# Kernel tuning notes

Measured on AMD Instinct MI355X. Metric: run time of the kernel, lower is better.

Reference implementation:

```python
import jax, jax.numpy as jnp
import numpy as np

FILTERS = 64
HIDDEN = 128
T_PRED = 24
DILATIONS = (1, 2, 4, 8, 16, 32)
N_DIL = len(DILATIONS)
FEAT = 15
B = 1024
L_ENC = 168


def setup_inputs() -> dict:
    key = jax.random.key(0)
    ks = jax.random.split(key, 16)
    s = 0.05
    d_in = 1 + FEAT  # prev_output (1) concat current feature
    inp = {
        "decoder_features": jax.random.normal(ks[0], (B, T_PRED, FEAT), jnp.float32),
        "decoder_init_input": jax.random.normal(ks[1], (B, 1), jnp.float32),
        "encoder_states": jax.random.normal(ks[2], (N_DIL, B, L_ENC, FILTERS), jnp.float32),
        # dense_1: d_in -> filters (tanh)
        "W1": jax.random.normal(ks[3], (d_in, FILTERS), jnp.float32) * s,
        "b1": jnp.zeros((FILTERS,), jnp.float32),
        # dense_2: filters -> 2*filters (bias)
        "W2": jax.random.normal(ks[4], (FILTERS, 2 * FILTERS), jnp.float32) * s,
        "b2": jnp.zeros((2 * FILTERS,), jnp.float32),
        # dense_3: filters -> 2*filters (no bias)
        "W3": jax.random.normal(ks[5], (FILTERS, 2 * FILTERS), jnp.float32) * s,
        # dense_4: filters -> 2*filters (bias)
        "W4": jax.random.normal(ks[6], (FILTERS, 2 * FILTERS), jnp.float32) * s,
        "b4": jnp.zeros((2 * FILTERS,), jnp.float32),
        # dense_5: n_dil*filters -> hidden (relu)
        "W5": jax.random.normal(ks[7], (N_DIL * FILTERS, HIDDEN), jnp.float32) * s,
        "b5": jnp.zeros((HIDDEN,), jnp.float32),
        # dense_6: hidden -> 1
        "W6": jax.random.normal(ks[8], (HIDDEN, 1), jnp.float32) * s,
        "b6": jnp.zeros((1,), jnp.float32),
    }
    return inp


def _decode(decoder_features, decoder_init_input, encoder_states,
            W1, b1, W2, b2, W3, W4, b4, W5, b5, W6, b6):
    L = encoder_states.shape[2]
    # 'appended' holds the inputs written back into each dilation's state
    # (the growing-concat part of encoder_states in the original loop).
    appended0 = jnp.zeros((N_DIL, decoder_features.shape[0], T_PRED, FILTERS),
                          dtype=decoder_features.dtype)

    def step(carry, t):
        prev, appended = carry
        cur = jnp.concatenate([prev, decoder_features[:, t, :]], axis=1)  # [B, 1+FEAT]
        inputs = jnp.tanh(cur @ W1 + b1)  # [B, F]
        skips_list = []
        for i, d in enumerate(DILATIONS):
            # grown-state read index is (L + t) - d; if t >= d it lands in the
            # appended region (step t-d), otherwise in the original encoder state.
            idx_app = jnp.clip(t - d, 0, T_PRED - 1)
            idx_orig = jnp.clip(L + t - d, 0, L - 1)
            st_app = jax.lax.dynamic_index_in_dim(appended[i], idx_app, axis=1, keepdims=False)
            st_orig = jax.lax.dynamic_index_in_dim(encoder_states[i], idx_orig, axis=1, keepdims=False)
            state = jnp.where(t >= d, st_app, st_orig)  # [B, F]
            dilated = state @ W2 + b2 + inputs @ W3  # [B, 2F]
            conv_filter, conv_gate = dilated[:, :FILTERS], dilated[:, FILTERS:]
            gated = jnp.tanh(conv_filter) * jax.nn.sigmoid(conv_gate)
            out = gated @ W4 + b4  # [B, 2F]
            skips, residuals = out[:, :FILTERS], out[:, FILTERS:]
            inputs = inputs + residuals
            appended = appended.at[i, :, t, :].set(inputs)
            skips_list.append(skips)
        skip = jax.nn.relu(jnp.concatenate(skips_list, axis=1))  # [B, N_DIL*F]
        h = jax.nn.relu(skip @ W5 + b5)
        y = h @ W6 + b6  # [B, 1]
        return (y, appended), y

    (_, _), ys = jax.lax.scan(step, (decoder_init_input, appended0),
                              jnp.arange(T_PRED))
    return jnp.transpose(ys, (1, 0, 2))  # [B, T, 1]


def reference(decoder_features, decoder_init_input, encoder_states,
              W1, b1, W2, b2, W3, W4, b4, W5, b5, W6, b6):
    return _decode(decoder_features, decoder_init_input, encoder_states,
                   W1, b1, W2, b2, W3, W4, b4, W5, b5, W6, b6)
```

## Files before the change

### kernel.cpp

```cpp
#include <hip/hip_runtime.h>

typedef _Float16 h16;
typedef _Float16 half4 __attribute__((ext_vector_type(4)));
typedef _Float16 half8 __attribute__((ext_vector_type(8)));
typedef float floatx4 __attribute__((ext_vector_type(4)));

#define B_TOT 1024
#define T_STEPS 24
#define F 64
#define C2 128
#define FEAT 15
#define L_ENC 168
#define HID 128
#define R 16
#define BLK 256
#define FP 72

__device__ __forceinline__ floatx4 mfma16(half8 a, half8 b, floatx4 c) {
  return __builtin_amdgcn_mfma_f32_16x16x32_f16(a, b, c, 0, 0, 0);
}

#define BAR() asm volatile("s_waitcnt lgkmcnt(0)\n\ts_barrier" ::: "memory")

__device__ __forceinline__ float tanh_fast(float x) {
  float cx = fminf(fmaxf(x, -15.f), 15.f);
  float e  = __builtin_amdgcn_exp2f(-2.885390081777927f * cx);
  return (1.f - e) * __builtin_amdgcn_rcpf(1.f + e);
}
__device__ __forceinline__ float gate_fast(float f, float g) {
  float cf = fminf(fmaxf(f, -15.f), 15.f);
  float cg = fminf(fmaxf(g, -30.f), 30.f);
  float ef = __builtin_amdgcn_exp2f(-2.885390081777927f * cf);
  float eg = __builtin_amdgcn_exp2f(-1.4426950408889634f * cg);
  return (1.f - ef) * __builtin_amdgcn_rcpf((1.f + ef) * (1.f + eg));
}

__global__ void prep_w5(const float* __restrict__ gW5, h16* __restrict__ wsW5) {
  int t = blockIdx.x * 256 + threadIdx.x;
  if (t >= 12 * 8 * 64) return;
  int lane = t & 63, nt = (t >> 6) & 7, ktg = t >> 9;
  int n  = nt * 16 + (lane & 15);
  int kb = ktg * 32 + (lane >> 4) * 8;
  half8 v;
  #pragma unroll
  for (int j = 0; j < 8; ++j) v[j] = (h16)gW5[(size_t)(kb + j) * C2 + n];
  *(half8*)&wsW5[(size_t)t * 8] = v;
}

__global__ __launch_bounds__(BLK, 1) void decoder_v9(
    const float* __restrict__ dec_feat,
    const float* __restrict__ dec_init,
    const float* __restrict__ enc,
    const float* __restrict__ gW1, const float* __restrict__ gb1,
    const float* __restrict__ gW2, const float* __restrict__ gb2,
    const float* __restrict__ gW3,
    const float* __restrict__ gW4, const float* __restrict__ gb4,
    const h16*  __restrict__ wsW5, const float* __restrict__ gb5,
    const float* __restrict__ gW6, const float* __restrict__ gb6,
    float* __restrict__ out)
{
  __shared__ alignas(16) h16 ringL[31][R][FP];
  __shared__ alignas(16) h16 enc5L[T_STEPS][R][FP];
  __shared__ alignas(16) h16 xH[R][FP];
  __shared__ alignas(16) h16 gatedH[R][FP];
  __shared__ alignas(16) h16 skipH[R][FP];
  __shared__ alignas(16) h16 featH[T_STEPS][R][16];
  __shared__ alignas(16) float ypartS[R][4];

  const int tid  = threadIdx.x;
  const int w    = tid >> 6;
  const int lane = tid & 63;
  const int m16  = lane & 15;
  const int q    = lane >> 4;
  const int q8   = q * 8;
  const int b0   = blockIdx.x * R;
  const int col  = w * 16 + m16;

  half8 rW1;
  #pragma unroll
  for (int j = 0; j < 8; ++j) {
    int k = q8 + j;
    rW1[j] = (k < 16) ? (h16)gW1[k * F + col] : (h16)0.0f;
  }
  half8 rW2[2][2], rW3[2][2], rW4[2][2];
  #pragma unroll
  for (int h = 0; h < 2; ++h) {
    int n = (w + 4 * h) * 16 + m16;
    #pragma unroll
    for (int kt = 0; kt < 2; ++kt) {
      half8 v2, v3, v4;
      #pragma unroll
      for (int j = 0; j < 8; ++j) {
        int k = kt * 32 + q8 + j;
        v2[j] = (h16)gW2[k * C2 + n];
        v3[j] = (h16)gW3[k * C2 + n];
        v4[j] = (h16)gW4[k * C2 + n];
      }
      rW2[h][kt] = v2; rW3[h][kt] = v3; rW4[h][kt] = v4;
    }
  }
  half8 w5r[6][4];
  #pragma unroll
  for (int i = 0; i < 6; ++i)
    #pragma unroll
    for (int kt = 0; kt < 2; ++kt)
      #pragma unroll
      for (int nn = 0; nn < 2; ++nn)
        w5r[i][kt * 2 + nn] =
            *(const half8*)&wsW5[(size_t)((((2 * i + kt) * 8) + (w + 4 * nn)) * 64 + lane) * 8];

  const float rb1  = gb1[col];
  const float rb2f = gb2[col], rb2g = gb2[64 + col];
  const float rb4s = gb4[col], rb4r = gb4[64 + col];
  const float rb5a = gb5[col], rb5b = gb5[64 + col];
  const float rw6a = gW6[col], rw6b = gW6[64 + col];
  const float rb6  = gb6[0];
  const float rInit = dec_init[b0 + m16];

  {
    int mm = tid >> 4, kk = (tid & 15) * 4;
    #pragma unroll 1
    for (int it = 0; it < 55; ++it) {
      int i, s; h16* dst;
      if (it < 31) {
        i = (it >= 15) ? 4 : (it >= 7) ? 3 : (it >= 3) ? 2 : (it >= 1) ? 1 : 0;
        s = it - ((1 << i) - 1);
        dst = &ringL[it][mm][kk];
      } else { i = 5; s = it - 31; dst = &enc5L[s][mm][kk]; }
      int d = 1 << i;
      const float* sp = enc + (((size_t)i * B_TOT + b0 + mm) * L_ENC + (L_ENC + s - d)) * F + kk;
      float4 v = *(const float4*)sp;
      half4 hv; hv[0] = (h16)v.x; hv[1] = (h16)v.y; hv[2] = (h16)v.z; hv[3] = (h16)v.w;
      *(half4*)dst = hv;
    }
  }
  for (int p = tid; p < T_STEPS * R; p += BLK) {
    int tt = p >> 4, row = p & 15;
    const float* sp = dec_feat + (size_t)(b0 + row) * (T_STEPS * FEAT) + tt * FEAT;
    half8 v0, v1;
    v0[0] = (h16)0.0f;
    #pragma unroll
    for (int j = 0; j < 7; ++j) v0[1 + j] = (h16)sp[j];
    #pragma unroll
    for (int j = 0; j < 8; ++j) v1[j] = (h16)sp[7 + j];
    *(half8*)&featH[tt][row][0] = v0;
    *(half8*)&featH[tt][row][8] = v1;
  }
  __syncthreads();

  auto loadStat = [&](half8* dst, int i, int t) {
    const h16* p;
    if (i == 5) p = &enc5L[t][m16][0];
    else {
      const int d = 1 << i;
      p = &ringL[((1 << i) - 1) + (t & (d - 1))][m16][0];
    }
    dst[0] = *(const half8*)(p + q8);
    dst[1] = *(const half8*)(p + 32 + q8);
  };

  float xr[4];

  for (int t = 0; t < T_STEPS; ++t) {
    float yv;
    if (t == 0) yv = rInit;
    else {
      float4 yp = *(const float4*)&ypartS[m16][0];
      yv = (yp.x + yp.y + yp.z + yp.w) + rb6;
    }
    if (t > 0 && w == 0 && q == 0)
      out[(size_t)(b0 + m16) * T_STEPS + (t - 1)] = yv;

    half8 aCur;
    if (q < 2) {
      aCur = *(const half8*)&featH[t][m16][q8];
    } else {
      #pragma unroll
      for (int j = 0; j < 8; ++j) aCur[j] = (h16)0.0f;
    }
    if (q == 0) aCur[0] = (h16)yv;
    floatx4 accX = {0.f, 0.f, 0.f, 0.f};
    accX = mfma16(aCur, rW1, accX);
    half8 stat[2];
    loadStat(stat, 0, t);
    #pragma unroll
    for (int j = 0; j < 4; ++j) {
      float v = tanh_fast(accX[j] + rb1);
      xr[j] = v;
      xH[q * 4 + j][col] = (h16)v;
    }
    BAR();

    floatx4 hAccA = {0.f, 0.f, 0.f, 0.f};
    floatx4 hAccB = {0.f, 0.f, 0.f, 0.f};

    #pragma unroll
    for (int i = 0; i < 6; ++i) {
      const int d = 1 << i;
      half8 xA0 = *(const half8*)&xH[m16][q8];
      half8 xA1 = *(const half8*)&xH[m16][32 + q8];
      half8 stN[2];
      if (i < 5) loadStat(stN, i + 1, t);

      floatx4 aF = {0.f, 0.f, 0.f, 0.f}, aG = {0.f, 0.f, 0.f, 0.f};
      aF = mfma16(stat[0], rW2[0][0], aF);
      aF = mfma16(stat[1], rW2[0][1], aF);
      aF = mfma16(xA0,     rW3[0][0], aF);
      aF = mfma16(xA1,     rW3[0][1], aF);
      aG = mfma16(stat[0], rW2[1][0], aG);
      aG = mfma16(stat[1], rW2[1][1], aG);
      aG = mfma16(xA0,     rW3[1][0], aG);
      aG = mfma16(xA1,     rW3[1][1], aG);
      #pragma unroll
      for (int j = 0; j < 4; ++j)
        gatedH[q * 4 + j][col] = (h16)gate_fast(aF[j] + rb2f, aG[j] + rb2g);
      BAR();

      half8 gA0 = *(const half8*)&gatedH[m16][q8];
      half8 gA1 = *(const half8*)&gatedH[m16][32 + q8];
      floatx4 oS = {0.f, 0.f, 0.f, 0.f}, oR = {0.f, 0.f, 0.f, 0.f};
      oS = mfma16(gA0, rW4[0][0], oS);
      oS = mfma16(gA1, rW4[0][1], oS);
      oR = mfma16(gA0, rW4[1][0], oR);
      oR = mfma16(gA1, rW4[1][1], oR);
      #pragma unroll
      for (int j = 0; j < 4; ++j) {
        int row = q * 4 + j;
        float s = oS[j] + rb4s;
        skipH[row][col] = (h16)fmaxf(s, 0.0f);
        float xn = xr[j] + oR[j] + rb4r;
        xr[j] = xn;
        h16 hx = (h16)xn;
        xH[row][col] = hx;
        if (i < 5) ringL[((1 << i) - 1) + (t & (d - 1))][row][col] = hx;
      }
      BAR();

      half8 sk0 = *(const half8*)&skipH[m16][q8];
      half8 sk1 = *(const half8*)&skipH[m16][32 + q8];
      hAccA = mfma16(sk0, w5r[i][0], hAccA);
      hAccA = mfma16(sk1, w5r[i][2], hAccA);
      hAccB = mfma16(sk0, w5r[i][1], hAccB);
      hAccB = mfma16(sk1, w5r[i][3], hAccB);

      if (i < 5) { stat[0] = stN[0]; stat[1] = stN[1]; }
    }

    {
      floatx4 vv;
      #pragma unroll
      for (int j = 0; j < 4; ++j) {
        float ha = fmaxf(hAccA[j] + rb5a, 0.0f);
        float hb = fmaxf(hAccB[j] + rb5b, 0.0f);
        vv[j] = ha * rw6a + hb * rw6b;
      }
      #pragma unroll
      for (int off = 1; off < 16; off <<= 1) {
        #pragma unroll
        for (int j = 0; j < 4; ++j) vv[j] += __shfl_xor(vv[j], off, 16);
      }
      if (m16 == 0) {
        #pragma unroll
        for (int j = 0; j < 4; ++j) ypartS[q * 4 + j][w] = vv[j];
      }
    }
    BAR();
  }

  {
    float4 yp = *(const float4*)&ypartS[m16][0];
    float yv = (yp.x + yp.y + yp.z + yp.w) + rb6;
    if (w == 0 && q == 0)
      out[(size_t)(b0 + m16) * T_STEPS + (T_STEPS - 1)] = yv;
  }
}

extern "C" void kernel_launch(void* const* d_in, const int* in_sizes, int n_in,
                              void* d_out, int out_size, void* d_ws, size_t ws_size,
                              hipStream_t stream) {
  const float* dec_feat = (const float*)d_in[0];
  const float* dec_init = (const float*)d_in[1];
  const float* enc      = (const float*)d_in[2];
  const float* W1 = (const float*)d_in[3];
  const float* b1 = (const float*)d_in[4];
  const float* W2 = (const float*)d_in[5];
  const float* b2 = (const float*)d_in[6];
  const float* W3 = (const float*)d_in[7];
  const float* W4 = (const float*)d_in[8];
  const float* b4 = (const float*)d_in[9];
  const float* W5 = (const float*)d_in[10];
  const float* b5 = (const float*)d_in[11];
  const float* W6 = (const float*)d_in[12];
  const float* b6 = (const float*)d_in[13];
  float* out = (float*)d_out;
  h16* wsW5 = (h16*)d_ws;

  prep_w5<<<24, 256, 0, stream>>>(W5, wsW5);
  decoder_v9<<<dim3(B_TOT / R), dim3(BLK), 0, stream>>>(
      dec_feat, dec_init, enc, W1, b1, W2, b2, W3, W4, b4, wsW5, b5, W6, b6, out);
}
```

Baseline: 447.2 us.

## Transpose MFMA operands so outputs are row-contiguous and vectorize LDS writes

Every MFMA now takes the weights as the A operand and the activations as B, so each lane holds four consecutive output columns for a single batch row. That lets the xH, gatedH, skipH and ring-buffer writes become half4 stores instead of scattered scalar stores, and bias vectors are loaded as float4. The dependent accumulation chains are split in two to expose more MFMA parallelism, and the final reduction drops from a 4-step 16-lane shuffle to two cross-quad shuffles. Weight registers are pinned with empty asm to stop them being rematerialized or spilled, at the cost of extra register pressure.

```diff
diff --git a/kernel.cpp b/kernel.cpp
--- a/kernel.cpp
+++ b/kernel.cpp
@@ -22,6 +22,8 @@
 
 #define BAR() asm volatile("s_waitcnt lgkmcnt(0)\n\ts_barrier" ::: "memory")
 
+#define PIN(x) asm volatile("" : "+v"(x))
+
 __device__ __forceinline__ float tanh_fast(float x) {
   float cx = fminf(fmaxf(x, -15.f), 15.f);
   float e  = __builtin_amdgcn_exp2f(-2.885390081777927f * cx);
@@ -47,7 +49,7 @@
   *(half8*)&wsW5[(size_t)t * 8] = v;
 }
 
-__global__ __launch_bounds__(BLK, 1) void decoder_v9(
+__global__ __launch_bounds__(BLK, 1) void decoder_v10(
     const float* __restrict__ dec_feat,
     const float* __restrict__ dec_init,
     const float* __restrict__ enc,
@@ -74,13 +76,13 @@
   const int q    = lane >> 4;
   const int q8   = q * 8;
   const int b0   = blockIdx.x * R;
-  const int col  = w * 16 + m16;
+  const int col4 = w * 16 + q * 4;
 
   half8 rW1;
   #pragma unroll
   for (int j = 0; j < 8; ++j) {
     int k = q8 + j;
-    rW1[j] = (k < 16) ? (h16)gW1[k * F + col] : (h16)0.0f;
+    rW1[j] = (k < 16) ? (h16)gW1[k * F + (w * 16 + m16)] : (h16)0.0f;
   }
   half8 rW2[2][2], rW3[2][2], rW4[2][2];
   #pragma unroll
@@ -109,12 +111,16 @@
         w5r[i][kt * 2 + nn] =
             *(const half8*)&wsW5[(size_t)((((2 * i + kt) * 8) + (w + 4 * nn)) * 64 + lane) * 8];
 
-  const float rb1  = gb1[col];
-  const float rb2f = gb2[col], rb2g = gb2[64 + col];
-  const float rb4s = gb4[col], rb4r = gb4[64 + col];
-  const float rb5a = gb5[col], rb5b = gb5[64 + col];
-  const float rw6a = gW6[col], rw6b = gW6[64 + col];
-  const float rb6  = gb6[0];
+  floatx4 rb1v  = *(const floatx4*)&gb1[col4];
+  floatx4 rb2fv = *(const floatx4*)&gb2[col4];
+  floatx4 rb2gv = *(const floatx4*)&gb2[64 + col4];
+  floatx4 rb4sv = *(const floatx4*)&gb4[col4];
+  floatx4 rb4rv = *(const floatx4*)&gb4[64 + col4];
+  floatx4 rb5av = *(const floatx4*)&gb5[col4];
+  floatx4 rb5bv = *(const floatx4*)&gb5[64 + col4];
+  floatx4 rw6av = *(const floatx4*)&gW6[col4];
+  floatx4 rw6bv = *(const floatx4*)&gW6[64 + col4];
+  const float rb6   = gb6[0];
   const float rInit = dec_init[b0 + m16];
 
   {
@@ -162,6 +168,18 @@
   float xr[4];
 
   for (int t = 0; t < T_STEPS; ++t) {
+    PIN(rW1);
+    #pragma unroll
+    for (int h = 0; h < 2; ++h)
+      #pragma unroll
+      for (int kt = 0; kt < 2; ++kt) { PIN(rW2[h][kt]); PIN(rW3[h][kt]); PIN(rW4[h][kt]); }
+    #pragma unroll
+    for (int i = 0; i < 6; ++i)
+      #pragma unroll
+      for (int k = 0; k < 4; ++k) PIN(w5r[i][k]);
+    PIN(rb1v); PIN(rb2fv); PIN(rb2gv); PIN(rb4sv); PIN(rb4rv);
+    PIN(rb5av); PIN(rb5bv); PIN(rw6av); PIN(rw6bv);
+
     float yv;
     if (t == 0) yv = rInit;
     else {
@@ -171,24 +189,26 @@
     if (t > 0 && w == 0 && q == 0)
       out[(size_t)(b0 + m16) * T_STEPS + (t - 1)] = yv;
 
-    half8 aCur;
+    half8 bCur;
     if (q < 2) {
-      aCur = *(const half8*)&featH[t][m16][q8];
+      bCur = *(const half8*)&featH[t][m16][q8];
     } else {
       #pragma unroll
-      for (int j = 0; j < 8; ++j) aCur[j] = (h16)0.0f;
-    }
-    if (q == 0) aCur[0] = (h16)yv;
+      for (int j = 0; j < 8; ++j) bCur[j] = (h16)0.0f;
+    }
+    if (q == 0) bCur[0] = (h16)yv;
     floatx4 accX = {0.f, 0.f, 0.f, 0.f};
-    accX = mfma16(aCur, rW1, accX);
+    accX = mfma16(rW1, bCur, accX);
     half8 stat[2];
     loadStat(stat, 0, t);
+    half4 xv;
     #pragma unroll
     for (int j = 0; j < 4; ++j) {
-      float v = tanh_fast(accX[j] + rb1);
+      float v = tanh_fast(accX[j] + rb1v[j]);
       xr[j] = v;
-      xH[q * 4 + j][col] = (h16)v;
-    }
+      xv[j] = (h16)v;
+    }
+    *(half4*)&xH[m16][col4] = xv;
     BAR();
 
     floatx4 hAccA = {0.f, 0.f, 0.f, 0.f};
@@ -197,72 +217,73 @@
     #pragma unroll
     for (int i = 0; i < 6; ++i) {
       const int d = 1 << i;
-      half8 xA0 = *(const half8*)&xH[m16][q8];
-      half8 xA1 = *(const half8*)&xH[m16][32 + q8];
+      half8 xB0 = *(const half8*)&xH[m16][q8];
+      half8 xB1 = *(const half8*)&xH[m16][32 + q8];
       half8 stN[2];
       if (i < 5) loadStat(stN, i + 1, t);
 
-      floatx4 aF = {0.f, 0.f, 0.f, 0.f}, aG = {0.f, 0.f, 0.f, 0.f};
-      aF = mfma16(stat[0], rW2[0][0], aF);
-      aF = mfma16(stat[1], rW2[0][1], aF);
-      aF = mfma16(xA0,     rW3[0][0], aF);
-      aF = mfma16(xA1,     rW3[0][1], aF);
-      aG = mfma16(stat[0], rW2[1][0], aG);
-      aG = mfma16(stat[1], rW2[1][1], aG);
-      aG = mfma16(xA0,     rW3[1][0], aG);
-      aG = mfma16(xA1,     rW3[1][1], aG);
-      #pragma unroll
-      for (int j = 0; j < 4; ++j)
-        gatedH[q * 4 + j][col] = (h16)gate_fast(aF[j] + rb2f, aG[j] + rb2g);
+      floatx4 aF0 = {0.f,0.f,0.f,0.f}, aF1 = {0.f,0.f,0.f,0.f};
+      floatx4 aG0 = {0.f,0.f,0.f,0.f}, aG1 = {0.f,0.f,0.f,0.f};
+      aF0 = mfma16(rW2[0][0], stat[0], aF0);
+      aF1 = mfma16(rW2[0][1], stat[1], aF1);
+      aG0 = mfma16(rW2[1][0], stat[0], aG0);
+      aG1 = mfma16(rW2[1][1], stat[1], aG1);
+      aF0 = mfma16(rW3[0][0], xB0, aF0);
+      aF1 = mfma16(rW3[0][1], xB1, aF1);
+      aG0 = mfma16(rW3[1][0], xB0, aG0);
+      aG1 = mfma16(rW3[1][1], xB1, aG1);
+      half4 gv;
+      #pragma unroll
+      for (int j = 0; j < 4; ++j) {
+        float f = aF0[j] + aF1[j] + rb2fv[j];
+        float g = aG0[j] + aG1[j] + rb2gv[j];
+        gv[j] = (h16)gate_fast(f, g);
+      }
+      *(half4*)&gatedH[m16][col4] = gv;
       BAR();
 
-      half8 gA0 = *(const half8*)&gatedH[m16][q8];
-      half8 gA1 = *(const half8*)&gatedH[m16][32 + q8];
-      floatx4 oS = {0.f, 0.f, 0.f, 0.f}, oR = {0.f, 0.f, 0.f, 0.f};
-      oS = mfma16(gA0, rW4[0][0], oS);
-      oS = mfma16(gA1, rW4[0][1], oS);
-      oR = mfma16(gA0, rW4[1][0], oR);
-      oR = mfma16(gA1, rW4[1][1], oR);
+      half8 gB0 = *(const half8*)&gatedH[m16][q8];
+      half8 gB1 = *(const half8*)&gatedH[m16][32 + q8];
+      floatx4 oS0 = {0.f,0.f,0.f,0.f}, oS1 = {0.f,0.f,0.f,0.f};
+      floatx4 oR0 = {0.f,0.f,0.f,0.f}, oR1 = {0.f,0.f,0.f,0.f};
+      oS0 = mfma16(rW4[0][0], gB0, oS0);
+      oS1 = mfma16(rW4[0][1], gB1, oS1);
+      oR0 = mfma16(rW4[1][0], gB0, oR0);
+      oR1 = mfma16(rW4[1][1], gB1, oR1);
+      half4 sv, xv2;
       #pragma unroll
       for (int j = 0; j < 4; ++j) {
-        int row = q * 4 + j;
-        float s = oS[j] + rb4s;
-        skipH[row][col] = (h16)fmaxf(s, 0.0f);
-        float xn = xr[j] + oR[j] + rb4r;
+        float s = oS0[j] + oS1[j] + rb4sv[j];
+        sv[j] = (h16)fmaxf(s, 0.0f);
+        float xn = xr[j] + (oR0[j] + oR1[j] + rb4rv[j]);
         xr[j] = xn;
-        h16 hx = (h16)xn;
-        xH[row][col] = hx;
-        if (i < 5) ringL[((1 << i) - 1) + (t & (d - 1))][row][col] = hx;
+        xv2[j] = (h16)xn;
       }
+      *(half4*)&skipH[m16][col4] = sv;
+      *(half4*)&xH[m16][col4]   = xv2;
+      if (i < 5) *(half4*)&ringL[((1 << i) - 1) + (t & (d - 1))][m16][col4] = xv2;
       BAR();
 
-      half8 sk0 = *(const half8*)&skipH[m16][q8];
-      half8 sk1 = *(const half8*)&skipH[m16][32 + q8];
-      hAccA = mfma16(sk0, w5r[i][0], hAccA);
-      hAccA = mfma16(sk1, w5r[i][2], hAccA);
-      hAccB = mfma16(sk0, w5r[i][1], hAccB);
-      hAccB = mfma16(sk1, w5r[i][3], hAccB);
+      half8 sB0 = *(const half8*)&skipH[m16][q8];
+      half8 sB1 = *(const half8*)&skipH[m16][32 + q8];
+      hAccA = mfma16(w5r[i][0], sB0, hAccA);
+      hAccA = mfma16(w5r[i][2], sB1, hAccA);
+      hAccB = mfma16(w5r[i][1], sB0, hAccB);
+      hAccB = mfma16(w5r[i][3], sB1, hAccB);
 
       if (i < 5) { stat[0] = stN[0]; stat[1] = stN[1]; }
     }
 
     {
-      floatx4 vv;
+      float vv = 0.f;
       #pragma unroll
       for (int j = 0; j < 4; ++j) {
-        float ha = fmaxf(hAccA[j] + rb5a, 0.0f);
-        float hb = fmaxf(hAccB[j] + rb5b, 0.0f);
-        vv[j] = ha * rw6a + hb * rw6b;
+        vv += fmaxf(hAccA[j] + rb5av[j], 0.0f) * rw6av[j];
+        vv += fmaxf(hAccB[j] + rb5bv[j], 0.0f) * rw6bv[j];
       }
-      #pragma unroll
-      for (int off = 1; off < 16; off <<= 1) {
-        #pragma unroll
-        for (int j = 0; j < 4; ++j) vv[j] += __shfl_xor(vv[j], off, 16);
-      }
-      if (m16 == 0) {
-        #pragma unroll
-        for (int j = 0; j < 4; ++j) ypartS[q * 4 + j][w] = vv[j];
-      }
+      vv += __shfl_xor(vv, 16);
+      vv += __shfl_xor(vv, 32);
+      if (q == 0) ypartS[m16][w] = vv;
     }
     BAR();
   }
@@ -296,6 +317,6 @@
   h16* wsW5 = (h16*)d_ws;
 
   prep_w5<<<24, 256, 0, stream>>>(W5, wsW5);
-  decoder_v9<<<dim3(B_TOT / R), dim3(BLK), 0, stream>>>(
+  decoder_v10<<<dim3(B_TOT / R), dim3(BLK), 0, stream>>>(
       dec_feat, dec_init, enc, W1, b1, W2, b2, W3, W4, b4, wsW5, b5, W6, b6, out);
 }
```

Result: no change. 440.7 us (-1.5%).
